# Kernel tuning notes

Measured on AMD Instinct MI355X. Metric: run time of the kernel, lower is better.

The kernel has to match this reference:

```python
import jax, jax.numpy as jnp
import numpy as np

HIDDEN = 512
E = 1024          # expansion: 2*hidden
S = 128           # qk dim
EPS = 1e-05
SQRT_S = float(np.sqrt(S))


def scale_norm(x, g):
    # ScaleNorm: x / max(||x|| * dim^-0.5, eps) * g
    norm = jnp.linalg.norm(x, axis=-1, keepdims=True) * (HIDDEN ** -0.5)
    return x / jnp.maximum(norm, EPS) * g


def rope(x):
    # x: [B, N, 2, S]; rotary over sequence dim (dim=1), kpt_structure=False
    n = x.shape[1]
    half = x.shape[-1] // 2
    position = jnp.arange(n, dtype=jnp.float32)            # [N]
    inv_freq = 10000.0 ** (jnp.arange(half, dtype=jnp.float32) / half)
    sinusoid = position[:, None, None] * inv_freq[None, None, :]  # [N,1,half]
    sin = jnp.sin(sinusoid)
    cos = jnp.cos(sinusoid)
    x1, x2 = jnp.split(x, 2, axis=-1)
    return jnp.concatenate([x1 * cos - x2 * sin, x2 * cos + x1 * sin], axis=-1)


def setup_inputs() -> dict:
    key = jax.random.key(0)
    ks = jax.random.split(key, 8)
    B, N = 32, 1024
    x = jax.random.normal(ks[0], (B, N, HIDDEN), dtype=jnp.float32)
    # xavier_uniform for uv weight
    fan_in, fan_out = HIDDEN, 2 * E + S
    bound = float(np.sqrt(6.0 / (fan_in + fan_out)))
    Wuv = jax.random.uniform(ks[1], (HIDDEN, 2 * E + S), minval=-bound, maxval=bound, dtype=jnp.float32)
    buv = jax.random.normal(ks[2], (2 * E + S,), dtype=jnp.float32) * 0.02
    gamma = jax.random.uniform(ks[3], (2, S), dtype=jnp.float32)
    beta = jax.random.uniform(ks[4], (2, S), dtype=jnp.float32)
    Wo = jax.random.normal(ks[5], (E, HIDDEN), dtype=jnp.float32) * (E ** -0.5)
    bo = jax.random.normal(ks[6], (HIDDEN,), dtype=jnp.float32) * 0.02
    g = jnp.ones((1,), dtype=jnp.float32)
    return {"x": x, "Wuv": Wuv, "buv": buv, "gamma": gamma, "beta": beta,
            "Wo": Wo, "bo": bo, "g": g}


def reference(x, Wuv, buv, gamma, beta, Wo, bo, g):
    shortcut = x                                   # use_shortcut (hidden==output)
    xn = scale_norm(x, g)
    uv = jax.nn.silu(xn @ Wuv + buv)               # [B,N,2e+s]
    u, v, base = jnp.split(uv, [E, 2 * E], axis=-1)
    # offset-scale: [B,N,S] -> [B,N,2,S]
    base = base[:, :, None, :] * gamma[None, None] + beta[None, None]
    base = rope(base)
    q = base[:, :, 0]                              # [B,N,S]
    k = base[:, :, 1]
    qk = jnp.einsum('bns,bms->bnm', q, k)          # [B,N,N]
    kernel = jnp.square(jax.nn.relu(qk / SQRT_S))  # relu2 attention kernel
    out = u * jnp.einsum('bnm,bme->bne', kernel, v)  # gated [B,N,E]
    return out @ Wo + bo + shortcut
```

## Files before the change

### kernel.cpp

```cpp
#include <hip/hip_runtime.h>
#include <cstdint>
#include <cstddef>

#define B_   32
#define N_   1024
#define H_   512
#define E_   1024
#define S_   128
#define NW_  2176
#define R_   (B_ * N_)

typedef unsigned short u16;
typedef __attribute__((ext_vector_type(8))) short bf16x8;
typedef __attribute__((ext_vector_type(4))) float f32x4;

static __device__ __forceinline__ float silu_f(float x) {
    return x / (1.0f + expf(-x));
}
static __device__ __forceinline__ u16 f2bf(float f) {
    unsigned u = __float_as_uint(f);
    unsigned r = u + 0x7fffu + ((u >> 16) & 1u);
    return (u16)(r >> 16);
}
static __device__ __forceinline__ float b2f(u16 h) {
    return __uint_as_float(((unsigned)h) << 16);
}

#define GLOAD_LDS16(SRC, DST)                                                  \
    __builtin_amdgcn_global_load_lds(                                          \
        (const __attribute__((address_space(1))) void*)(SRC),                  \
        (__attribute__((address_space(3))) void*)(DST), 16, 0, 0)

__device__ __forceinline__ void mm_tile_core(
    const u16* __restrict__ Atile, const u16* __restrict__ Btile,
    int KP, u16* As, u16* Bs, f32x4 acc[4][4])
{
    const int tid  = threadIdx.x;
    const int lane = tid & 63, wid = tid >> 6;
    const int wr = wid >> 1, wc = wid & 1;
    const int trow = tid >> 3;
    const int p    = (tid & 7) * 16;

    for (int kt = 0; kt < KP; kt += 64) {
        #pragma unroll
        for (int s = 0; s < 4; s++) {
            const int row = s * 32 + trow;
            const int kb  = p ^ ((row & 7) << 4);
            GLOAD_LDS16(Atile + (size_t)row * KP + kt + (kb >> 1),
                        (char*)As + s * 4096 + wid * 1024);
            GLOAD_LDS16(Btile + (size_t)row * KP + kt + (kb >> 1),
                        (char*)Bs + s * 4096 + wid * 1024);
        }
        __syncthreads();
        #pragma unroll
        for (int kk = 0; kk < 2; kk++) {
            const int kbyte = kk * 64 + (lane >> 4) * 16;
            bf16x8 af[4], bf[4];
            #pragma unroll
            for (int f = 0; f < 4; f++) {
                const int ra = wr * 64 + f * 16 + (lane & 15);
                af[f] = *(const bf16x8*)((const char*)As + ra * 128 +
                                         (kbyte ^ ((ra & 7) << 4)));
                const int rb = wc * 64 + f * 16 + (lane & 15);
                bf[f] = *(const bf16x8*)((const char*)Bs + rb * 128 +
                                         (kbyte ^ ((rb & 7) << 4)));
            }
            #pragma unroll
            for (int i = 0; i < 4; i++)
                #pragma unroll
                for (int j = 0; j < 4; j++)
                    acc[i][j] = __builtin_amdgcn_mfma_f32_16x16x32_bf16(
                        af[i], bf[j], acc[i][j], 0, 0, 0);
        }
        __syncthreads();
    }
}

__global__ __launch_bounds__(256) void scale_kernel(
    const float* __restrict__ x, const float* __restrict__ g,
    float* __restrict__ s)
{
    int row  = blockIdx.x * 4 + (threadIdx.x >> 6);
    int lane = threadIdx.x & 63;
    const float4* xr = (const float4*)(x + (size_t)row * H_);
    float4 a = xr[lane];
    float4 b = xr[lane + 64];
    float acc = a.x*a.x + a.y*a.y + a.z*a.z + a.w*a.w
              + b.x*b.x + b.y*b.y + b.z*b.z + b.w*b.w;
    #pragma unroll
    for (int off = 1; off < 64; off <<= 1)
        acc += __shfl_xor(acc, off);
    if (lane == 0) {
        float norm = sqrtf(acc) * 0.044194173824159216f;
        s[row] = g[0] / fmaxf(norm, 1e-5f);
    }
}

__global__ __launch_bounds__(256) void trig_kernel(
    float* __restrict__ sin_t, float* __restrict__ cos_t)
{
    int idx = blockIdx.x * 256 + threadIdx.x;
    int n = idx >> 6;
    int i = idx & 63;
    double invf_d = pow(10000.0, (double)i * (1.0 / 64.0));
    float  invf   = (float)invf_d;
    float  arg    = (float)n * invf;
    sin_t[idx] = (float)sin((double)arg);
    cos_t[idx] = (float)cos((double)arg);
}

__global__ __launch_bounds__(256) void xnp_kernel(
    const float* __restrict__ x, const float* __restrict__ s,
    u16* __restrict__ xnP)
{
    int idx = blockIdx.x * 256 + threadIdx.x;
    int r = idx >> 9, k = idx & 511;
    float v = x[(size_t)r * H_ + k] * s[r];
    u16 h = f2bf(v), l = f2bf(v - b2f(h));
    u16* xr = xnP + (size_t)r * 1536;
    xr[k] = h; xr[512 + k] = h; xr[1024 + k] = l;
}

__global__ __launch_bounds__(256) void wuvt_kernel(
    const float* __restrict__ Wuv, u16* __restrict__ WuvT)
{
    int k = blockIdx.x;
    for (int c = threadIdx.x; c < NW_; c += 256) {
        float v = Wuv[(size_t)k * NW_ + c];
        u16 h = f2bf(v), l = f2bf(v - b2f(h));
        u16* wr = WuvT + (size_t)c * 1536;
        wr[k] = h; wr[512 + k] = l; wr[1024 + k] = h;
    }
}

__global__ __launch_bounds__(256) void wot_kernel(
    const float* __restrict__ Wo, u16* __restrict__ WoT)
{
    int k = blockIdx.x;
    for (int c = threadIdx.x; c < H_; c += 256) {
        float v = Wo[(size_t)k * H_ + c];
        u16 h = f2bf(v), l = f2bf(v - b2f(h));
        u16* wr = WoT + (size_t)c * 3072;
        wr[k] = h; wr[1024 + k] = l; wr[2048 + k] = h;
    }
}

__global__ __launch_bounds__(256) void gemm1_mfma(
    const u16* __restrict__ xnP, const u16* __restrict__ WuvT,
    const float* __restrict__ buv,
    float* __restrict__ u, u16* __restrict__ vT, float* __restrict__ qb)
{
    __shared__ u16 As[128 * 64];
    __shared__ u16 Bs[128 * 64];
    f32x4 acc[4][4];
    #pragma unroll
    for (int i = 0; i < 4; i++)
        #pragma unroll
        for (int j = 0; j < 4; j++) acc[i][j] = (f32x4){0.f, 0.f, 0.f, 0.f};

    mm_tile_core(xnP + (size_t)blockIdx.x * 128 * 1536,
                 WuvT + (size_t)blockIdx.y * 128 * 1536, 1536, As, Bs, acc);

    const int lane = threadIdx.x & 63, wid = threadIdx.x >> 6;
    const int wr = wid >> 1, wc = wid & 1;
    const int r0 = (lane >> 4) * 4, c0 = lane & 15;
    #pragma unroll
    for (int i = 0; i < 4; i++) {
        #pragma unroll
        for (int j = 0; j < 4; j++) {
            const int col = blockIdx.y * 128 + wc * 64 + j * 16 + c0;
            const float bc = buv[col];
            #pragma unroll
            for (int r = 0; r < 4; r++) {
                const int row = blockIdx.x * 128 + wr * 64 + i * 16 + r0 + r;
                float val = silu_f(acc[i][j][r] + bc);
                if (col < E_) {
                    u[(size_t)row * E_ + col] = val;
                } else if (col < 2 * E_) {
                    const int e = col - E_, b = row >> 10, m = row & (N_ - 1);
                    u16 h = f2bf(val), l = f2bf(val - b2f(h));
                    u16* vr = vT + ((size_t)b * N_ + e) * 3072;
                    vr[m] = h; vr[1024 + m] = l; vr[2048 + m] = h;
                } else {
                    qb[(size_t)row * S_ + (col - 2 * E_)] = val;
                }
            }
        }
    }
}

__global__ __launch_bounds__(256) void rope_kernel(
    float* __restrict__ qb, float* __restrict__ kb,
    const float* __restrict__ gamma, const float* __restrict__ beta,
    const float* __restrict__ sin_t, const float* __restrict__ cos_t)
{
    int row = blockIdx.x * 4 + (threadIdx.x >> 6);
    int i   = threadIdx.x & 63;
    int n   = row & (N_ - 1);
    size_t base = (size_t)row * S_;
    float b1 = qb[base + i];
    float b2 = qb[base + i + 64];
    float sn = sin_t[n * 64 + i];
    float cs = cos_t[n * 64 + i];
    float t1 = b1 * gamma[i]      + beta[i];
    float t2 = b2 * gamma[i + 64] + beta[i + 64];
    qb[base + i]      = t1 * cs - t2 * sn;
    qb[base + i + 64] = t2 * cs + t1 * sn;
    t1 = b1 * gamma[128 + i]      + beta[128 + i];
    t2 = b2 * gamma[128 + i + 64] + beta[128 + i + 64];
    kb[base + i]      = t1 * cs - t2 * sn;
    kb[base + i + 64] = t2 * cs + t1 * sn;
}

__global__ __launch_bounds__(256) void qk_kernel(
    const float* __restrict__ q, const float* __restrict__ k,
    u16* __restrict__ Aq)
{
    __shared__ float Qs[8][128];
    __shared__ float Ks[8][128];
    const int tid = threadIdx.x;
    const int bm = blockIdx.x, bn = blockIdx.y, b = blockIdx.z;
    const int tx = tid & 15, ty = tid >> 4;
    const int arow = tid >> 1, ak = (tid & 1) * 4;
    const float* Qp = q + (size_t)b * N_ * S_ + (size_t)(bm * 128 + arow) * S_ + ak;
    const float* Kp = k + (size_t)b * N_ * S_ + (size_t)(bn * 128 + arow) * S_ + ak;

    float acc[8][8];
    #pragma unroll
    for (int i = 0; i < 8; i++)
        #pragma unroll
        for (int j = 0; j < 8; j++) acc[i][j] = 0.0f;

    float4 a4 = *(const float4*)(Qp);
    float4 b4 = *(const float4*)(Kp);
    for (int kt = 0; kt < S_; kt += 8) {
        Qs[ak + 0][arow] = a4.x; Qs[ak + 1][arow] = a4.y;
        Qs[ak + 2][arow] = a4.z; Qs[ak + 3][arow] = a4.w;
        Ks[ak + 0][arow] = b4.x; Ks[ak + 1][arow] = b4.y;
        Ks[ak + 2][arow] = b4.z; Ks[ak + 3][arow] = b4.w;
        __syncthreads();
        const int ktn = (kt + 8 < S_) ? kt + 8 : kt;
        float4 a4n = *(const float4*)(Qp + ktn);
        float4 b4n = *(const float4*)(Kp + ktn);
        #pragma unroll
        for (int kk = 0; kk < 8; kk++) {
            float a[8], bb[8];
            *(float4*)&a[0]  = *(const float4*)&Qs[kk][ty * 8];
            *(float4*)&a[4]  = *(const float4*)&Qs[kk][ty * 8 + 4];
            *(float4*)&bb[0] = *(const float4*)&Ks[kk][tx * 8];
            *(float4*)&bb[4] = *(const float4*)&Ks[kk][tx * 8 + 4];
            #pragma unroll
            for (int i = 0; i < 8; i++)
                #pragma unroll
                for (int j = 0; j < 8; j++)
                    acc[i][j] += a[i] * bb[j];
        }
        __syncthreads();
        a4 = a4n; b4 = b4n;
    }

    const int row0 = bm * 128 + ty * 8;
    const int col0 = bn * 128 + tx * 8;
    u16* Ab = Aq + (size_t)b * N_ * 3072;
    #pragma unroll
    for (int i = 0; i < 8; i++) {
        u16* ar = Ab + (size_t)(row0 + i) * 3072;
        #pragma unroll
        for (int j = 0; j < 8; j++) {
            float t = acc[i][j] / 11.313708498984761f;
            t = fmaxf(t, 0.0f);
            t = t * t;
            u16 h = f2bf(t), l = f2bf(t - b2f(h));
            ar[col0 + j] = h; ar[1024 + col0 + j] = h; ar[2048 + col0 + j] = l;
        }
    }
}

__global__ __launch_bounds__(256) void av_mfma(
    const u16* __restrict__ Aq, const u16* __restrict__ vT,
    const float* __restrict__ u, u16* __restrict__ yP)
{
    __shared__ u16 As[128 * 64];
    __shared__ u16 Bs[128 * 64];
    f32x4 acc[4][4];
    #pragma unroll
    for (int i = 0; i < 4; i++)
        #pragma unroll
        for (int j = 0; j < 4; j++) acc[i][j] = (f32x4){0.f, 0.f, 0.f, 0.f};

    const int b = blockIdx.z;
    mm_tile_core(Aq + ((size_t)b * N_ + blockIdx.x * 128) * 3072,
                 vT + ((size_t)b * N_ + blockIdx.y * 128) * 3072, 3072,
                 As, Bs, acc);

    const int lane = threadIdx.x & 63, wid = threadIdx.x >> 6;
    const int wr = wid >> 1, wc = wid & 1;
    const int r0 = (lane >> 4) * 4, c0 = lane & 15;
    #pragma unroll
    for (int i = 0; i < 4; i++) {
        #pragma unroll
        for (int j = 0; j < 4; j++) {
            const int e = blockIdx.y * 128 + wc * 64 + j * 16 + c0;
            #pragma unroll
            for (int r = 0; r < 4; r++) {
                const int row = blockIdx.x * 128 + wr * 64 + i * 16 + r0 + r;
                const size_t gr = (size_t)b * N_ + row;
                float y = u[gr * E_ + e] * acc[i][j][r];
                u16 h = f2bf(y), l = f2bf(y - b2f(h));
                u16* yr = yP + gr * 3072;
                yr[e] = h; yr[1024 + e] = h; yr[2048 + e] = l;
            }
        }
    }
}

__global__ __launch_bounds__(256) void final_mfma(
    const u16* __restrict__ yP, const u16* __restrict__ WoT,
    const float* __restrict__ bo, const float* __restrict__ x,
    float* __restrict__ out)
{
    __shared__ u16 As[128 * 64];
    __shared__ u16 Bs[128 * 64];
    f32x4 acc[4][4];
    #pragma unroll
    for (int i = 0; i < 4; i++)
        #pragma unroll
        for (int j = 0; j < 4; j++) acc[i][j] = (f32x4){0.f, 0.f, 0.f, 0.f};

    mm_tile_core(yP + (size_t)blockIdx.x * 128 * 3072,
                 WoT + (size_t)blockIdx.y * 128 * 3072, 3072, As, Bs, acc);

    const int lane = threadIdx.x & 63, wid = threadIdx.x >> 6;
    const int wr = wid >> 1, wc = wid & 1;
    const int r0 = (lane >> 4) * 4, c0 = lane & 15;
    #pragma unroll
    for (int i = 0; i < 4; i++) {
        #pragma unroll
        for (int j = 0; j < 4; j++) {
            const int col = blockIdx.y * 128 + wc * 64 + j * 16 + c0;
            const float bc = bo[col];
            #pragma unroll
            for (int r = 0; r < 4; r++) {
                const int row = blockIdx.x * 128 + wr * 64 + i * 16 + r0 + r;
                out[(size_t)row * H_ + col] =
                    acc[i][j][r] + bc + x[(size_t)row * H_ + col];
            }
        }
    }
}

extern "C" void kernel_launch(void* const* d_in, const int* in_sizes, int n_in,
                              void* d_out, int out_size, void* d_ws, size_t ws_size,
                              hipStream_t stream)
{
    const float* x     = (const float*)d_in[0];
    const float* Wuv   = (const float*)d_in[1];
    const float* buv   = (const float*)d_in[2];
    const float* gamma = (const float*)d_in[3];
    const float* beta  = (const float*)d_in[4];
    const float* Wo    = (const float*)d_in[5];
    const float* bo    = (const float*)d_in[6];
    const float* g     = (const float*)d_in[7];
    float* out = (float*)d_out;

    const size_t fixedB = (size_t)R_ * 4 + 2 * 65536 * 4
                        + (size_t)NW_ * 1536 * 2
                        + (size_t)H_ * 3072 * 2;
    const size_t perBatchB = 27262976ull;
    int c = 8;
    while (c > 1) {
        if (fixedB + (size_t)c * perBatchB <= ws_size) break;
        c >>= 1;
    }
    const int Rc = c * N_;

    char* p = (char*)d_ws;
    float* s_buf = (float*)p;  p += (size_t)R_ * 4;
    float* sin_t = (float*)p;  p += (size_t)N_ * 64 * 4;
    float* cos_t = (float*)p;  p += (size_t)N_ * 64 * 4;
    u16*   WuvT  = (u16*)p;    p += (size_t)NW_ * 1536 * 2;
    u16*   WoT   = (u16*)p;    p += (size_t)H_ * 3072 * 2;
    u16*   xnP   = (u16*)p;    p += (size_t)Rc * 1536 * 2;
    float* qb    = (float*)p;  p += (size_t)Rc * S_ * 4;
    float* kb    = (float*)p;  p += (size_t)Rc * S_ * 4;
    float* u_c   = (float*)p;  p += (size_t)Rc * E_ * 4;
    u16*   vT    = (u16*)p;    p += (size_t)Rc * 3072 * 2;
    u16*   Aq    = (u16*)p;    p += (size_t)Rc * 3072 * 2;
    u16*   yP    = (u16*)p;    p += (size_t)Rc * 3072 * 2;

    scale_kernel<<<R_ / 4, 256, 0, stream>>>(x, g, s_buf);
    trig_kernel<<<(N_ * 64) / 256, 256, 0, stream>>>(sin_t, cos_t);
    wuvt_kernel<<<H_, 256, 0, stream>>>(Wuv, WuvT);
    wot_kernel<<<E_, 256, 0, stream>>>(Wo, WoT);

    for (int b0 = 0; b0 < B_; b0 += c) {
        const size_t ro = (size_t)b0 * N_;
        xnp_kernel<<<(Rc * 512) / 256, 256, 0, stream>>>(
            x + ro * H_, s_buf + ro, xnP);
        gemm1_mfma<<<dim3(Rc / 128, NW_ / 128), 256, 0, stream>>>(
            xnP, WuvT, buv, u_c, vT, qb);
        rope_kernel<<<Rc / 4, 256, 0, stream>>>(
            qb, kb, gamma, beta, sin_t, cos_t);
        qk_kernel<<<dim3(N_ / 128, N_ / 128, c), 256, 0, stream>>>(
            qb, kb, Aq);
        av_mfma<<<dim3(N_ / 128, N_ / 128, c), 256, 0, stream>>>(
            Aq, vT, u_c, yP);
        final_mfma<<<dim3(Rc / 128, H_ / 128), 256, 0, stream>>>(
            yP, WoT, bo, x + ro * H_, out + ro * H_);
    }
}
```

Measured before the change: 1.596 ms.

## Double-buffer LDS tiles in shared MFMA GEMM core to overlap loads

Converts the shared GEMM tile loop to double buffering. The next K-slice is issued via global_load_lds into the alternate LDS buffer while MFMAs run on the current one, hiding global load latency behind compute. LDS use per block doubles to 64 KB, which may lower occupancy. Correctness depends on the compiler waiting for the async LDS loads before the barrier.

```diff
diff --git a/kernel.cpp b/kernel.cpp
--- a/kernel.cpp
+++ b/kernel.cpp
@@ -31,6 +31,19 @@
         (const __attribute__((address_space(1))) void*)(SRC),                  \
         (__attribute__((address_space(3))) void*)(DST), 16, 0, 0)
 
+#define STAGE(BUF, KT)                                                         \
+    {                                                                          \
+        _Pragma("unroll")                                                      \
+        for (int s = 0; s < 4; s++) {                                          \
+            const int row = s * 32 + trow;                                     \
+            const int kb  = p ^ ((row & 7) << 4);                              \
+            GLOAD_LDS16(Atile + (size_t)row * KP + (KT) + (kb >> 1),           \
+                        (char*)As + (BUF) * 16384 + s * 4096 + wid * 1024);    \
+            GLOAD_LDS16(Btile + (size_t)row * KP + (KT) + (kb >> 1),           \
+                        (char*)Bs + (BUF) * 16384 + s * 4096 + wid * 1024);    \
+        }                                                                      \
+    }
+
 __device__ __forceinline__ void mm_tile_core(
     const u16* __restrict__ Atile, const u16* __restrict__ Btile,
     int KP, u16* As, u16* Bs, f32x4 acc[4][4])
@@ -41,17 +54,13 @@
     const int trow = tid >> 3;
     const int p    = (tid & 7) * 16;
 
+    STAGE(0, 0);
+    __syncthreads();
+    int cur = 0;
     for (int kt = 0; kt < KP; kt += 64) {
-        #pragma unroll
-        for (int s = 0; s < 4; s++) {
-            const int row = s * 32 + trow;
-            const int kb  = p ^ ((row & 7) << 4);
-            GLOAD_LDS16(Atile + (size_t)row * KP + kt + (kb >> 1),
-                        (char*)As + s * 4096 + wid * 1024);
-            GLOAD_LDS16(Btile + (size_t)row * KP + kt + (kb >> 1),
-                        (char*)Bs + s * 4096 + wid * 1024);
-        }
-        __syncthreads();
+        if (kt + 64 < KP) STAGE(cur ^ 1, kt + 64);
+        const char* Ab = (const char*)As + cur * 16384;
+        const char* Bb = (const char*)Bs + cur * 16384;
         #pragma unroll
         for (int kk = 0; kk < 2; kk++) {
             const int kbyte = kk * 64 + (lane >> 4) * 16;
@@ -59,10 +68,10 @@
             #pragma unroll
             for (int f = 0; f < 4; f++) {
                 const int ra = wr * 64 + f * 16 + (lane & 15);
-                af[f] = *(const bf16x8*)((const char*)As + ra * 128 +
+                af[f] = *(const bf16x8*)(Ab + ra * 128 +
                                          (kbyte ^ ((ra & 7) << 4)));
                 const int rb = wc * 64 + f * 16 + (lane & 15);
-                bf[f] = *(const bf16x8*)((const char*)Bs + rb * 128 +
+                bf[f] = *(const bf16x8*)(Bb + rb * 128 +
                                          (kbyte ^ ((rb & 7) << 4)));
             }
             #pragma unroll
@@ -73,6 +82,7 @@
                         af[i], bf[j], acc[i][j], 0, 0, 0);
         }
         __syncthreads();
+        cur ^= 1;
     }
 }
 
@@ -150,8 +160,8 @@
     const float* __restrict__ buv,
     float* __restrict__ u, u16* __restrict__ vT, float* __restrict__ qb)
 {
-    __shared__ u16 As[128 * 64];
-    __shared__ u16 Bs[128 * 64];
+    __shared__ u16 As[2 * 128 * 64];
+    __shared__ u16 Bs[2 * 128 * 64];
     f32x4 acc[4][4];
     #pragma unroll
     for (int i = 0; i < 4; i++)
@@ -280,8 +290,8 @@
     const u16* __restrict__ Aq, const u16* __restrict__ vT,
     const float* __restrict__ u, u16* __restrict__ yP)
 {
-    __shared__ u16 As[128 * 64];
-    __shared__ u16 Bs[128 * 64];
+    __shared__ u16 As[2 * 128 * 64];
+    __shared__ u16 Bs[2 * 128 * 64];
     f32x4 acc[4][4];
     #pragma unroll
     for (int i = 0; i < 4; i++)
@@ -319,8 +329,8 @@
     const float* __restrict__ bo, const float* __restrict__ x,
     float* __restrict__ out)
 {
-    __shared__ u16 As[128 * 64];
-    __shared__ u16 Bs[128 * 64];
+    __shared__ u16 As[2 * 128 * 64];
+    __shared__ u16 Bs[2 * 128 * 64];
     f32x4 acc[4][4];
     #pragma unroll
     for (int i = 0; i < 4; i++)
```

New measurement: 1.561 ms. 2.2% less time.
